# Kernel tuning notes

Measured on AMD Instinct MI355X. Metric: run time of the kernel, lower is better.

Reference implementation:

```python
import jax, jax.numpy as jnp
import numpy as np

N = 50000      # nodes
E = 800000     # edges
F = 256        # input features (glove identity)
H = 64         # hidden dim of GCN stack
C = 16         # num classes
PE = 200000    # pos/neg edges each

@jax.custom_vjp
def grad_reverse(x):
    return x

def _gr_fwd(x):
    return x, None

def _gr_bwd(_, g):
    return (-g,)

grad_reverse.defvjp(_gr_fwd, _gr_bwd)

def _gcn_norm(edge_index, n):
    # add self loops + symmetric normalization (PyG GCNConv default)
    loops = jnp.arange(n, dtype=edge_index.dtype)
    src = jnp.concatenate([edge_index[0], loops])
    dst = jnp.concatenate([edge_index[1], loops])
    deg = jax.ops.segment_sum(jnp.ones(src.shape, jnp.float32), dst, num_segments=n)
    dinv = jnp.where(deg > 0, jax.lax.rsqrt(jnp.maximum(deg, 1.0)), 0.0)
    return src, dst, dinv[src] * dinv[dst]

def _gcn(x, W, b, src, dst, norm, n):
    h = x @ W                                   # [n, out]
    msg = h[src] * norm[:, None]                # gather + edge scale
    return jax.ops.segment_sum(msg, dst, num_segments=n) + b

def setup_inputs():
    key = jax.random.key(0)
    ks = jax.random.split(key, 14)
    s = 0.05
    return {
        "input": jax.random.normal(ks[0], (N, F), jnp.float32),
        "glove": jnp.eye(F, dtype=jnp.float32),
        "W1": jax.random.normal(ks[1], (F, H), jnp.float32) * s,
        "b1": jnp.zeros((H,), jnp.float32),
        "W2": jax.random.normal(ks[2], (H, H), jnp.float32) * s,
        "b2": jnp.zeros((H,), jnp.float32),
        "W3": jax.random.normal(ks[3], (H, H), jnp.float32) * s,
        "b3": jnp.zeros((H,), jnp.float32),
        "Wa": jax.random.normal(ks[4], (H, C), jnp.float32) * s,
        "ba": jnp.zeros((C,), jnp.float32),
        "Wk": jax.random.normal(ks[5], (H, C), jnp.float32) * s,
        "bk": jnp.zeros((C,), jnp.float32),
        "edge_index": jax.random.randint(ks[6], (2, E), 0, N, dtype=jnp.int32),
        "pos_edge_index": jax.random.randint(ks[7], (2, PE), 0, N, dtype=jnp.int32),
        "neg_edge_index": jax.random.randint(ks[8], (2, PE), 0, N, dtype=jnp.int32),
    }

def reference(input, glove, W1, b1, W2, b2, W3, b3, Wa, ba, Wk, bk,
              edge_index, pos_edge_index, neg_edge_index):
    src, dst, norm = _gcn_norm(edge_index, N)
    x = input @ glove
    x = jax.nn.relu(_gcn(x, W1, b1, src, dst, norm, N))
    x = _gcn(x, W2, b2, src, dst, norm, N)
    x = _gcn(x, W3, b3, src, dst, norm, N)
    feat = x
    attr = _gcn(x, Wa, ba, src, dst, norm, N)
    att = _gcn(grad_reverse(x), Wk, bk, src, dst, norm, N)
    tei = jnp.concatenate([pos_edge_index, neg_edge_index], axis=-1)  # [2, 2*PE]
    x_j = x[tei[0]]
    x_i = x[tei[1]]
    res = jnp.einsum('ef,ef->e', x_i, x_j)
    return res, jax.nn.log_softmax(attr, axis=1), att, feat
```

## Files before the change

### kernel.cpp

```cpp
#include <hip/hip_runtime.h>
#include <hip/hip_bf16.h>

#define N_NODES 50000
#define N_EDGES 800000
#define F_IN    256
#define H_DIM   64
#define C_DIM   16
#define PE_CNT  200000

typedef __hip_bfloat16 bf16;

__device__ __forceinline__ float b2f(bf16 v) { return __bfloat162float(v); }
__device__ __forceinline__ bf16  f2b(float v) { return __float2bfloat16(v); }


__global__ void hist_build_kernel(const int* __restrict__ dst, int* __restrict__ hist,
                                  const float* __restrict__ Wa, const float* __restrict__ Wk,
                                  float* __restrict__ Wh) {
    int e = blockIdx.x * blockDim.x + threadIdx.x;
    if (e < N_EDGES) atomicAdd(&hist[dst[e]], 1);
    if (blockIdx.x == 0) {
        for (int idx = threadIdx.x; idx < H_DIM * 32; idx += 256) {
            int f = idx >> 5, c = idx & 31;
            Wh[idx] = (c < C_DIM) ? Wa[f * C_DIM + c] : Wk[f * C_DIM + (c - C_DIM)];
        }
    }
}

__global__ __launch_bounds__(1024) void scan_block_kernel(const int* __restrict__ hist,
                                                          int* __restrict__ excl,
                                                          int* __restrict__ partials) {
    __shared__ int buf[1024];
    int i = blockIdx.x * 1024 + threadIdx.x;
    int v = (i < N_NODES) ? hist[i] : 0;
    buf[threadIdx.x] = v;
    __syncthreads();
    for (int off = 1; off < 1024; off <<= 1) {
        int t = (threadIdx.x >= off) ? buf[threadIdx.x - off] : 0;
        __syncthreads();
        buf[threadIdx.x] += t;
        __syncthreads();
    }
    int incl = buf[threadIdx.x];
    if (i < N_NODES) excl[i] = incl - v;
    if (threadIdx.x == 1023) partials[blockIdx.x] = incl;
}

__global__ void scan_partials_kernel(int* __restrict__ partials) {
    int t = threadIdx.x;
    int orig = (t < 49) ? partials[t] : 0;
    int v = orig;
    for (int off = 1; off < 64; off <<= 1) {
        int u = __shfl_up(v, off, 64);
        if (t >= off) v += u;
    }
    if (t < 49) partials[t] = v - orig;
}

__global__ void scan_add_kernel(int* __restrict__ rowstart, const int* __restrict__ partials,
                                int* __restrict__ cursor, const int* __restrict__ hist,
                                float* __restrict__ dinv) {
    int i = blockIdx.x * blockDim.x + threadIdx.x;
    if (i < N_NODES) {
        int v = rowstart[i] + partials[i >> 10];
        rowstart[i] = v;
        cursor[i]   = v;
        dinv[i]     = rsqrtf((float)(hist[i] + 1));
    } else if (i == N_NODES) {
        rowstart[i] = N_EDGES;
    }
}

__global__ void scatter_kernel(const int* __restrict__ ei, int* __restrict__ cursor,
                               const float* __restrict__ dinv, int2* __restrict__ csr2) {
    int e = blockIdx.x * blockDim.x + threadIdx.x;
    if (e < N_EDGES) {
        int s = ei[e];
        int d = ei[N_EDGES + e];
        int p = atomicAdd(&cursor[d], 1);
        csr2[p] = make_int2(s, __float_as_int(dinv[s]));
    }
}

#define G_ROWS 32
#define G_KCH  64
#define XS_LD  68

__global__ __launch_bounds__(256) void gemm_k256_kernel(const float* __restrict__ x,
                                                        const float* __restrict__ W,
                                                        bf16* __restrict__ h1) {
    __shared__ float xs[G_ROWS * XS_LD];
    __shared__ float ws[G_KCH * H_DIM];
    int t = threadIdx.x;
    int row0 = blockIdx.x * G_ROWS;
    int col = t & 63;
    int wv  = t >> 6;

    float acc[8];
#pragma unroll
    for (int i = 0; i < 8; i++) acc[i] = 0.f;

    for (int c = 0; c < F_IN / G_KCH; c++) {
        int k0 = c * G_KCH;
        {
            const float4* Wg = (const float4*)(W + k0 * H_DIM);
            float4* wl = (float4*)ws;
#pragma unroll
            for (int i = 0; i < 4; i++) wl[t + 256 * i] = Wg[t + 256 * i];
        }
        {
            int r = t >> 3;
            int jj = (t & 7) * 8;
            int row = row0 + r;
            float4 v0 = make_float4(0.f, 0.f, 0.f, 0.f), v1 = v0;
            if (row < N_NODES) {
                const float4* xg = (const float4*)(x + (size_t)row * F_IN + k0 + jj);
                v0 = xg[0];
                v1 = xg[1];
            }
            float4* xl = (float4*)&xs[r * XS_LD + jj];
            xl[0] = v0;
            xl[1] = v1;
        }
        __syncthreads();
#pragma unroll 4
        for (int kk = 0; kk < G_KCH; kk += 4) {
            float w0 = ws[(kk + 0) * H_DIM + col];
            float w1 = ws[(kk + 1) * H_DIM + col];
            float w2 = ws[(kk + 2) * H_DIM + col];
            float w3 = ws[(kk + 3) * H_DIM + col];
#pragma unroll
            for (int i = 0; i < 8; i++) {
                float4 xv = *(const float4*)&xs[(wv * 8 + i) * XS_LD + kk];
                acc[i] += xv.x * w0 + xv.y * w1 + xv.z * w2 + xv.w * w3;
            }
        }
        __syncthreads();
    }
#pragma unroll
    for (int i = 0; i < 8; i++) {
        int row = row0 + wv * 8 + i;
        if (row < N_NODES) h1[(size_t)row * H_DIM + col] = f2b(acc[i]);
    }
}

template <int RELU>
__global__ __launch_bounds__(256) void agg_gemm_kernel(const bf16* __restrict__ h,
                                                       const int* __restrict__ rowstart,
                                                       const int2* __restrict__ csr2,
                                                       const float* __restrict__ dinv,
                                                       const float* __restrict__ bagg,
                                                       const float* __restrict__ W,
                                                       bf16* __restrict__ hnext) {
    int lane = threadIdx.x & 63;
    int node = blockIdx.x * 4 + __builtin_amdgcn_readfirstlane(threadIdx.x >> 6);
    float dn = dinv[node];
    int s0 = rowstart[node], s1 = rowstart[node + 1];
    float acc0 = dn * b2f(h[(size_t)node * H_DIM + lane]);
    float acc1 = 0.f;
    int j = s0;
    for (; j + 1 < s1; j += 2) {
        int2 e0 = csr2[j], e1 = csr2[j + 1];
        acc0 += __int_as_float(e0.y) * b2f(h[(size_t)e0.x * H_DIM + lane]);
        acc1 += __int_as_float(e1.y) * b2f(h[(size_t)e1.x * H_DIM + lane]);
    }
    if (j < s1) {
        int2 e0 = csr2[j];
        acc0 += __int_as_float(e0.y) * b2f(h[(size_t)e0.x * H_DIM + lane]);
    }
    float v = dn * (acc0 + acc1) + bagg[lane];
    if (RELU) v = fmaxf(v, 0.f);
    float o = 0.f;
#pragma unroll
    for (int f = 0; f < H_DIM; f++) {
        float vf = __shfl(v, f, 64);
        o += vf * W[f * H_DIM + lane];
    }
    hnext[(size_t)node * H_DIM + lane] = f2b(o);
}

__global__ __launch_bounds__(256) void agg_out_kernel(const bf16* __restrict__ h,
                                                      const int* __restrict__ rowstart,
                                                      const int2* __restrict__ csr2,
                                                      const float* __restrict__ dinv,
                                                      const float* __restrict__ b3,
                                                      float* __restrict__ feat,
                                                      bf16* __restrict__ featb) {
    int lane = threadIdx.x & 63;
    int node = blockIdx.x * 4 + __builtin_amdgcn_readfirstlane(threadIdx.x >> 6);
    float dn = dinv[node];
    int s0 = rowstart[node], s1 = rowstart[node + 1];
    float acc0 = dn * b2f(h[(size_t)node * H_DIM + lane]);
    float acc1 = 0.f;
    int j = s0;
    for (; j + 1 < s1; j += 2) {
        int2 e0 = csr2[j], e1 = csr2[j + 1];
        acc0 += __int_as_float(e0.y) * b2f(h[(size_t)e0.x * H_DIM + lane]);
        acc1 += __int_as_float(e1.y) * b2f(h[(size_t)e1.x * H_DIM + lane]);
    }
    if (j < s1) {
        int2 e0 = csr2[j];
        acc0 += __int_as_float(e0.y) * b2f(h[(size_t)e0.x * H_DIM + lane]);
    }
    float v = dn * (acc0 + acc1) + b3[lane];
    feat[(size_t)node * H_DIM + lane]  = v;
    featb[(size_t)node * H_DIM + lane] = f2b(v);
}

__global__ __launch_bounds__(256) void head_kernel(const bf16* __restrict__ featb,
                                                   const int* __restrict__ rowstart,
                                                   const int2* __restrict__ csr2,
                                                   const float* __restrict__ dinv,
                                                   const float* __restrict__ Wh,
                                                   const float* __restrict__ ba,
                                                   const float* __restrict__ bk,
                                                   float* __restrict__ lsm,
                                                   float* __restrict__ att) {
    int lane = threadIdx.x & 63;
    int node = blockIdx.x * 4 + __builtin_amdgcn_readfirstlane(threadIdx.x >> 6);
    float dn = dinv[node];
    int s0 = rowstart[node], s1 = rowstart[node + 1];
    float acc0 = dn * b2f(featb[(size_t)node * H_DIM + lane]);
    float acc1 = 0.f;
    int j = s0;
    for (; j + 1 < s1; j += 2) {
        int2 e0 = csr2[j], e1 = csr2[j + 1];
        acc0 += __int_as_float(e0.y) * b2f(featb[(size_t)e0.x * H_DIM + lane]);
        acc1 += __int_as_float(e1.y) * b2f(featb[(size_t)e1.x * H_DIM + lane]);
    }
    if (j < s1) {
        int2 e0 = csr2[j];
        acc0 += __int_as_float(e0.y) * b2f(featb[(size_t)e0.x * H_DIM + lane]);
    }
    float y = dn * (acc0 + acc1);

    int c32 = lane & 31;
    int fbase = lane & 32;
    float part = 0.f;
#pragma unroll
    for (int i = 0; i < 32; i++) {
        float yf = __shfl(y, fbase + i, 64);
        part += yf * Wh[(fbase + i) * 32 + c32];
    }
    float full = part + __shfl(part, lane ^ 32, 64);
    if (lane < 32) {
        float bias = (lane < C_DIM) ? ba[lane] : bk[lane - C_DIM];
        float hv = full + bias;
        if (lane < C_DIM) {
            float m = hv;
#pragma unroll
            for (int off = 1; off < 16; off <<= 1) m = fmaxf(m, __shfl_xor(m, off, 64));
            float e = __expf(hv - m);
            float sum = e;
#pragma unroll
            for (int off = 1; off < 16; off <<= 1) sum += __shfl_xor(sum, off, 64);
            lsm[(size_t)node * C_DIM + lane] = (hv - m) - __logf(sum);
        } else {
            att[(size_t)node * C_DIM + (lane - C_DIM)] = hv;
        }
    }
}

__global__ __launch_bounds__(256) void edge_dot_kernel(const int* __restrict__ pos,
                                                       const int* __restrict__ neg,
                                                       const bf16* __restrict__ xb,
                                                       float* __restrict__ res) {
    int e = blockIdx.x * 16 + (threadIdx.x >> 4);
    int lane = threadIdx.x & 15;
    int a, b;
    if (e < PE_CNT) {
        a = pos[e];
        b = pos[PE_CNT + e];
    } else {
        int e2 = e - PE_CNT;
        a = neg[e2];
        b = neg[PE_CNT + e2];
    }
    uint2 ua = ((const uint2*)(xb + (size_t)a * H_DIM))[lane];
    uint2 ub = ((const uint2*)(xb + (size_t)b * H_DIM))[lane];
    float a0 = __uint_as_float(ua.x << 16), a1 = __uint_as_float(ua.x & 0xffff0000u);
    float a2 = __uint_as_float(ua.y << 16), a3 = __uint_as_float(ua.y & 0xffff0000u);
    float b0 = __uint_as_float(ub.x << 16), b1 = __uint_as_float(ub.x & 0xffff0000u);
    float b2 = __uint_as_float(ub.y << 16), b3 = __uint_as_float(ub.y & 0xffff0000u);
    float acc = a0 * b0 + a1 * b1 + a2 * b2 + a3 * b3;
#pragma unroll
    for (int off = 1; off < 16; off <<= 1) acc += __shfl_xor(acc, off, 64);
    if (lane == 0) res[e] = acc;
}


extern "C" void kernel_launch(void* const* d_in, const int* in_sizes, int n_in,
                              void* d_out, int out_size, void* d_ws, size_t ws_size,
                              hipStream_t stream) {
    const float* input = (const float*)d_in[0];
    const float* W1 = (const float*)d_in[2];
    const float* b1 = (const float*)d_in[3];
    const float* W2 = (const float*)d_in[4];
    const float* b2 = (const float*)d_in[5];
    const float* W3 = (const float*)d_in[6];
    const float* b3 = (const float*)d_in[7];
    const float* Wa = (const float*)d_in[8];
    const float* ba = (const float*)d_in[9];
    const float* Wk = (const float*)d_in[10];
    const float* bk = (const float*)d_in[11];
    const int* ei  = (const int*)d_in[12];
    const int* pos = (const int*)d_in[13];
    const int* neg = (const int*)d_in[14];

    char* ws = (char*)d_ws;
    int*   hist     = (int*)(ws + 0);
    int*   rowstart = (int*)(ws + 200704);
    int*   cursor   = (int*)(ws + 401408);
    float* dinv     = (float*)(ws + 602112);
    int*   partials = (int*)(ws + 802816);
    float* Wh       = (float*)(ws + 803072);
    int2*  csr2     = (int2*)(ws + 811264);
    bf16*  bufA     = (bf16*)(ws + 7211264ULL);
    bf16*  bufB     = (bf16*)(ws + 13611264ULL);

    float* out  = (float*)d_out;
    float* res  = out;
    float* lsm  = out + 400000;
    float* att  = out + 1200000;
    float* feat = out + 2000000;

    hipMemsetAsync(hist, 0, N_NODES * sizeof(int), stream);
    hist_build_kernel<<<(N_EDGES + 255) / 256, 256, 0, stream>>>(ei + N_EDGES, hist, Wa, Wk, Wh);
    scan_block_kernel<<<49, 1024, 0, stream>>>(hist, rowstart, partials);
    scan_partials_kernel<<<1, 64, 0, stream>>>(partials);
    scan_add_kernel<<<196, 256, 0, stream>>>(rowstart, partials, cursor, hist, dinv);
    scatter_kernel<<<(N_EDGES + 255) / 256, 256, 0, stream>>>(ei, cursor, dinv, csr2);

    gemm_k256_kernel<<<(N_NODES + G_ROWS - 1) / G_ROWS, 256, 0, stream>>>(input, W1, bufA);
    agg_gemm_kernel<1><<<12500, 256, 0, stream>>>(bufA, rowstart, csr2, dinv, b1, W2, bufB);
    agg_gemm_kernel<0><<<12500, 256, 0, stream>>>(bufB, rowstart, csr2, dinv, b2, W3, bufA);
    agg_out_kernel<<<12500, 256, 0, stream>>>(bufA, rowstart, csr2, dinv, b3, feat, bufB);
    head_kernel<<<12500, 256, 0, stream>>>(bufB, rowstart, csr2, dinv, Wh, ba, bk, lsm, att);
    edge_dot_kernel<<<25000, 256, 0, stream>>>(pos, neg, bufB, res);
}
```

Measured before the change: 437.0 us.

## Project features before head aggregation, retile GEMM, vectorize gathers and edge dots

Moves the head's 64->32 projection ahead of the final aggregation, so the head kernel gathers 32-wide bf16 rows instead of 64-wide ones and handles two nodes per wavefront. The first GEMM is retiled to a 2x4 register tile per thread with float4 shared-memory reads and packed bf16 stores. Aggregation loops are unrolled by four with paired 128-bit CSR loads, and W is staged in shared memory. The edge dot kernel uses 128-bit loads with 8 lanes per edge. In exchange it adds a bf16 rounding of the projected features and an extra intermediate buffer.

```diff
diff --git a/kernel.cpp b/kernel.cpp
--- a/kernel.cpp
+++ b/kernel.cpp
@@ -12,6 +12,9 @@
 
 __device__ __forceinline__ float b2f(bf16 v) { return __bfloat162float(v); }
 __device__ __forceinline__ bf16  f2b(float v) { return __float2bfloat16(v); }
+__device__ __forceinline__ unsigned short f2b_u(float v) {
+    union { bf16 b; unsigned short u; } cv; cv.b = __float2bfloat16(v); return cv.u;
+}
 
 
 __global__ void hist_build_kernel(const int* __restrict__ dst, int* __restrict__ hist,
@@ -82,6 +85,29 @@
     }
 }
 
+#define AGG_BODY(TBL, STRIDE, CIDX)                                                      \
+    float acc0 = dn * b2f(TBL[(size_t)node * STRIDE + CIDX]);                            \
+    float acc1 = 0.f, acc2 = 0.f, acc3 = 0.f;                                            \
+    int j = s0;                                                                          \
+    if ((j & 1) && j < s1) {                                                             \
+        int2 e = csr2[j];                                                                \
+        acc1 += __int_as_float(e.y) * b2f(TBL[(size_t)e.x * STRIDE + CIDX]);             \
+        j++;                                                                             \
+    }                                                                                    \
+    for (; j + 3 < s1; j += 4) {                                                         \
+        int4 p01 = *(const int4*)&csr2[j];                                               \
+        int4 p23 = *(const int4*)&csr2[j + 2];                                           \
+        acc0 += __int_as_float(p01.y) * b2f(TBL[(size_t)p01.x * STRIDE + CIDX]);         \
+        acc1 += __int_as_float(p01.w) * b2f(TBL[(size_t)p01.z * STRIDE + CIDX]);         \
+        acc2 += __int_as_float(p23.y) * b2f(TBL[(size_t)p23.x * STRIDE + CIDX]);         \
+        acc3 += __int_as_float(p23.w) * b2f(TBL[(size_t)p23.z * STRIDE + CIDX]);         \
+    }                                                                                    \
+    for (; j < s1; j++) {                                                                \
+        int2 e = csr2[j];                                                                \
+        acc0 += __int_as_float(e.y) * b2f(TBL[(size_t)e.x * STRIDE + CIDX]);             \
+    }                                                                                    \
+    float aggsum = (acc0 + acc1) + (acc2 + acc3);
+
 #define G_ROWS 32
 #define G_KCH  64
 #define XS_LD  68
@@ -93,12 +119,11 @@
     __shared__ float ws[G_KCH * H_DIM];
     int t = threadIdx.x;
     int row0 = blockIdx.x * G_ROWS;
-    int col = t & 63;
-    int wv  = t >> 6;
-
-    float acc[8];
-#pragma unroll
-    for (int i = 0; i < 8; i++) acc[i] = 0.f;
+    int c4 = (t & 15) * 4;
+    int r2 = (t >> 4) * 2;
+
+    float acc00 = 0.f, acc01 = 0.f, acc02 = 0.f, acc03 = 0.f;
+    float acc10 = 0.f, acc11 = 0.f, acc12 = 0.f, acc13 = 0.f;
 
     for (int c = 0; c < F_IN / G_KCH; c++) {
         int k0 = c * G_KCH;
@@ -109,8 +134,7 @@
             for (int i = 0; i < 4; i++) wl[t + 256 * i] = Wg[t + 256 * i];
         }
         {
-            int r = t >> 3;
-            int jj = (t & 7) * 8;
+            int r = t >> 3, jj = (t & 7) * 8;
             int row = row0 + r;
             float4 v0 = make_float4(0.f, 0.f, 0.f, 0.f), v1 = v0;
             if (row < N_NODES) {
@@ -123,24 +147,33 @@
             xl[1] = v1;
         }
         __syncthreads();
-#pragma unroll 4
+#pragma unroll 8
         for (int kk = 0; kk < G_KCH; kk += 4) {
-            float w0 = ws[(kk + 0) * H_DIM + col];
-            float w1 = ws[(kk + 1) * H_DIM + col];
-            float w2 = ws[(kk + 2) * H_DIM + col];
-            float w3 = ws[(kk + 3) * H_DIM + col];
-#pragma unroll
-            for (int i = 0; i < 8; i++) {
-                float4 xv = *(const float4*)&xs[(wv * 8 + i) * XS_LD + kk];
-                acc[i] += xv.x * w0 + xv.y * w1 + xv.z * w2 + xv.w * w3;
-            }
+            float4 xv0 = *(const float4*)&xs[(r2 + 0) * XS_LD + kk];
+            float4 xv1 = *(const float4*)&xs[(r2 + 1) * XS_LD + kk];
+            float4 w0 = *(const float4*)&ws[(kk + 0) * H_DIM + c4];
+            float4 w1 = *(const float4*)&ws[(kk + 1) * H_DIM + c4];
+            float4 w2 = *(const float4*)&ws[(kk + 2) * H_DIM + c4];
+            float4 w3 = *(const float4*)&ws[(kk + 3) * H_DIM + c4];
+            acc00 += xv0.x * w0.x + xv0.y * w1.x + xv0.z * w2.x + xv0.w * w3.x;
+            acc01 += xv0.x * w0.y + xv0.y * w1.y + xv0.z * w2.y + xv0.w * w3.y;
+            acc02 += xv0.x * w0.z + xv0.y * w1.z + xv0.z * w2.z + xv0.w * w3.z;
+            acc03 += xv0.x * w0.w + xv0.y * w1.w + xv0.z * w2.w + xv0.w * w3.w;
+            acc10 += xv1.x * w0.x + xv1.y * w1.x + xv1.z * w2.x + xv1.w * w3.x;
+            acc11 += xv1.x * w0.y + xv1.y * w1.y + xv1.z * w2.y + xv1.w * w3.y;
+            acc12 += xv1.x * w0.z + xv1.y * w1.z + xv1.z * w2.z + xv1.w * w3.z;
+            acc13 += xv1.x * w0.w + xv1.y * w1.w + xv1.z * w2.w + xv1.w * w3.w;
         }
         __syncthreads();
     }
-#pragma unroll
-    for (int i = 0; i < 8; i++) {
-        int row = row0 + wv * 8 + i;
-        if (row < N_NODES) h1[(size_t)row * H_DIM + col] = f2b(acc[i]);
+    int rowA = row0 + r2, rowB = rowA + 1;
+    if (rowA < N_NODES) {
+        ushort4 p = make_ushort4(f2b_u(acc00), f2b_u(acc01), f2b_u(acc02), f2b_u(acc03));
+        *(ushort4*)&h1[(size_t)rowA * H_DIM + c4] = p;
+    }
+    if (rowB < N_NODES) {
+        ushort4 p = make_ushort4(f2b_u(acc10), f2b_u(acc11), f2b_u(acc12), f2b_u(acc13));
+        *(ushort4*)&h1[(size_t)rowB * H_DIM + c4] = p;
     }
 }
 
@@ -152,30 +185,26 @@
                                                        const float* __restrict__ bagg,
                                                        const float* __restrict__ W,
                                                        bf16* __restrict__ hnext) {
-    int lane = threadIdx.x & 63;
-    int node = blockIdx.x * 4 + __builtin_amdgcn_readfirstlane(threadIdx.x >> 6);
+    __shared__ float Wl[H_DIM * H_DIM];
+    int t = threadIdx.x;
+    {
+        const float4* Wg = (const float4*)W;
+        float4* wl = (float4*)Wl;
+#pragma unroll
+        for (int i = 0; i < 4; i++) wl[t + 256 * i] = Wg[t + 256 * i];
+    }
+    __syncthreads();
+    int lane = t & 63;
+    int node = blockIdx.x * 4 + __builtin_amdgcn_readfirstlane(t >> 6);
     float dn = dinv[node];
     int s0 = rowstart[node], s1 = rowstart[node + 1];
-    float acc0 = dn * b2f(h[(size_t)node * H_DIM + lane]);
-    float acc1 = 0.f;
-    int j = s0;
-    for (; j + 1 < s1; j += 2) {
-        int2 e0 = csr2[j], e1 = csr2[j + 1];
-        acc0 += __int_as_float(e0.y) * b2f(h[(size_t)e0.x * H_DIM + lane]);
-        acc1 += __int_as_float(e1.y) * b2f(h[(size_t)e1.x * H_DIM + lane]);
-    }
-    if (j < s1) {
-        int2 e0 = csr2[j];
-        acc0 += __int_as_float(e0.y) * b2f(h[(size_t)e0.x * H_DIM + lane]);
-    }
-    float v = dn * (acc0 + acc1) + bagg[lane];
+    AGG_BODY(h, H_DIM, lane)
+    float v = dn * aggsum + bagg[lane];
     if (RELU) v = fmaxf(v, 0.f);
     float o = 0.f;
 #pragma unroll
-    for (int f = 0; f < H_DIM; f++) {
-        float vf = __shfl(v, f, 64);
-        o += vf * W[f * H_DIM + lane];
-    }
+    for (int f = 0; f < H_DIM; f++)
+        o += __shfl(v, f, 64) * Wl[f * H_DIM + lane];
     hnext[(size_t)node * H_DIM + lane] = f2b(o);
 }
 
@@ -184,80 +213,66 @@
                                                       const int2* __restrict__ csr2,
                                                       const float* __restrict__ dinv,
                                                       const float* __restrict__ b3,
+                                                      const float* __restrict__ Wh,
                                                       float* __restrict__ feat,
-                                                      bf16* __restrict__ featb) {
-    int lane = threadIdx.x & 63;
-    int node = blockIdx.x * 4 + __builtin_amdgcn_readfirstlane(threadIdx.x >> 6);
+                                                      bf16* __restrict__ featb,
+                                                      bf16* __restrict__ zb) {
+    __shared__ float Whs[H_DIM * 32];
+    int t = threadIdx.x;
+    {
+        const float4* Wg = (const float4*)Wh;
+        float4* wl = (float4*)Whs;
+#pragma unroll
+        for (int i = 0; i < 2; i++) wl[t + 256 * i] = Wg[t + 256 * i];
+    }
+    __syncthreads();
+    int lane = t & 63;
+    int node = blockIdx.x * 4 + __builtin_amdgcn_readfirstlane(t >> 6);
     float dn = dinv[node];
     int s0 = rowstart[node], s1 = rowstart[node + 1];
-    float acc0 = dn * b2f(h[(size_t)node * H_DIM + lane]);
-    float acc1 = 0.f;
-    int j = s0;
-    for (; j + 1 < s1; j += 2) {
-        int2 e0 = csr2[j], e1 = csr2[j + 1];
-        acc0 += __int_as_float(e0.y) * b2f(h[(size_t)e0.x * H_DIM + lane]);
-        acc1 += __int_as_float(e1.y) * b2f(h[(size_t)e1.x * H_DIM + lane]);
-    }
-    if (j < s1) {
-        int2 e0 = csr2[j];
-        acc0 += __int_as_float(e0.y) * b2f(h[(size_t)e0.x * H_DIM + lane]);
-    }
-    float v = dn * (acc0 + acc1) + b3[lane];
+    AGG_BODY(h, H_DIM, lane)
+    float v = dn * aggsum + b3[lane];
     feat[(size_t)node * H_DIM + lane]  = v;
     featb[(size_t)node * H_DIM + lane] = f2b(v);
-}
-
-__global__ __launch_bounds__(256) void head_kernel(const bf16* __restrict__ featb,
+    int c32 = lane & 31;
+    float zc = 0.f;
+#pragma unroll
+    for (int f = 0; f < H_DIM; f++)
+        zc += __shfl(v, f, 64) * Whs[f * 32 + c32];
+    if (lane < 32) zb[(size_t)node * 32 + lane] = f2b(zc);
+}
+
+__global__ __launch_bounds__(256) void head_kernel(const bf16* __restrict__ zb,
                                                    const int* __restrict__ rowstart,
                                                    const int2* __restrict__ csr2,
                                                    const float* __restrict__ dinv,
-                                                   const float* __restrict__ Wh,
                                                    const float* __restrict__ ba,
                                                    const float* __restrict__ bk,
                                                    float* __restrict__ lsm,
                                                    float* __restrict__ att) {
-    int lane = threadIdx.x & 63;
-    int node = blockIdx.x * 4 + __builtin_amdgcn_readfirstlane(threadIdx.x >> 6);
+    int t = threadIdx.x;
+    int lane = t & 63;
+    int half = lane >> 5;
+    int c32 = lane & 31;
+    int wid = __builtin_amdgcn_readfirstlane(t >> 6);
+    int node = blockIdx.x * 8 + wid * 2 + half;
     float dn = dinv[node];
     int s0 = rowstart[node], s1 = rowstart[node + 1];
-    float acc0 = dn * b2f(featb[(size_t)node * H_DIM + lane]);
-    float acc1 = 0.f;
-    int j = s0;
-    for (; j + 1 < s1; j += 2) {
-        int2 e0 = csr2[j], e1 = csr2[j + 1];
-        acc0 += __int_as_float(e0.y) * b2f(featb[(size_t)e0.x * H_DIM + lane]);
-        acc1 += __int_as_float(e1.y) * b2f(featb[(size_t)e1.x * H_DIM + lane]);
-    }
-    if (j < s1) {
-        int2 e0 = csr2[j];
-        acc0 += __int_as_float(e0.y) * b2f(featb[(size_t)e0.x * H_DIM + lane]);
-    }
-    float y = dn * (acc0 + acc1);
-
-    int c32 = lane & 31;
-    int fbase = lane & 32;
-    float part = 0.f;
-#pragma unroll
-    for (int i = 0; i < 32; i++) {
-        float yf = __shfl(y, fbase + i, 64);
-        part += yf * Wh[(fbase + i) * 32 + c32];
-    }
-    float full = part + __shfl(part, lane ^ 32, 64);
-    if (lane < 32) {
-        float bias = (lane < C_DIM) ? ba[lane] : bk[lane - C_DIM];
-        float hv = full + bias;
-        if (lane < C_DIM) {
-            float m = hv;
-#pragma unroll
-            for (int off = 1; off < 16; off <<= 1) m = fmaxf(m, __shfl_xor(m, off, 64));
-            float e = __expf(hv - m);
-            float sum = e;
-#pragma unroll
-            for (int off = 1; off < 16; off <<= 1) sum += __shfl_xor(sum, off, 64);
-            lsm[(size_t)node * C_DIM + lane] = (hv - m) - __logf(sum);
-        } else {
-            att[(size_t)node * C_DIM + (lane - C_DIM)] = hv;
-        }
+    AGG_BODY(zb, 32, c32)
+    float y = dn * aggsum;
+    int c = c32 & 15;
+    float hv = y + ((c32 < 16) ? ba[c] : bk[c]);
+    if (c32 < 16) {
+        float m = hv;
+#pragma unroll
+        for (int off = 1; off < 16; off <<= 1) m = fmaxf(m, __shfl_xor(m, off, 64));
+        float e = __expf(hv - m);
+        float sum = e;
+#pragma unroll
+        for (int off = 1; off < 16; off <<= 1) sum += __shfl_xor(sum, off, 64);
+        lsm[(size_t)node * C_DIM + c] = (hv - m) - __logf(sum);
+    } else {
+        att[(size_t)node * C_DIM + c] = hv;
     }
 }
 
@@ -265,8 +280,8 @@
                                                        const int* __restrict__ neg,
                                                        const bf16* __restrict__ xb,
                                                        float* __restrict__ res) {
-    int e = blockIdx.x * 16 + (threadIdx.x >> 4);
-    int lane = threadIdx.x & 15;
+    int e = blockIdx.x * 32 + (threadIdx.x >> 3);
+    int lane8 = threadIdx.x & 7;
     int a, b;
     if (e < PE_CNT) {
         a = pos[e];
@@ -276,16 +291,29 @@
         a = neg[e2];
         b = neg[PE_CNT + e2];
     }
-    uint2 ua = ((const uint2*)(xb + (size_t)a * H_DIM))[lane];
-    uint2 ub = ((const uint2*)(xb + (size_t)b * H_DIM))[lane];
-    float a0 = __uint_as_float(ua.x << 16), a1 = __uint_as_float(ua.x & 0xffff0000u);
-    float a2 = __uint_as_float(ua.y << 16), a3 = __uint_as_float(ua.y & 0xffff0000u);
-    float b0 = __uint_as_float(ub.x << 16), b1 = __uint_as_float(ub.x & 0xffff0000u);
-    float b2 = __uint_as_float(ub.y << 16), b3 = __uint_as_float(ub.y & 0xffff0000u);
-    float acc = a0 * b0 + a1 * b1 + a2 * b2 + a3 * b3;
-#pragma unroll
-    for (int off = 1; off < 16; off <<= 1) acc += __shfl_xor(acc, off, 64);
-    if (lane == 0) res[e] = acc;
+    uint4 ua = ((const uint4*)(xb + (size_t)a * H_DIM))[lane8];
+    uint4 ub = ((const uint4*)(xb + (size_t)b * H_DIM))[lane8];
+    float acc;
+    {
+        float s = 0.f;
+        unsigned au, bu;
+        au = ua.x; bu = ub.x;
+        s += __uint_as_float(au << 16) * __uint_as_float(bu << 16);
+        s += __uint_as_float(au & 0xffff0000u) * __uint_as_float(bu & 0xffff0000u);
+        au = ua.y; bu = ub.y;
+        s += __uint_as_float(au << 16) * __uint_as_float(bu << 16);
+        s += __uint_as_float(au & 0xffff0000u) * __uint_as_float(bu & 0xffff0000u);
+        au = ua.z; bu = ub.z;
+        s += __uint_as_float(au << 16) * __uint_as_float(bu << 16);
+        s += __uint_as_float(au & 0xffff0000u) * __uint_as_float(bu & 0xffff0000u);
+        au = ua.w; bu = ub.w;
+        s += __uint_as_float(au << 16) * __uint_as_float(bu << 16);
+        s += __uint_as_float(au & 0xffff0000u) * __uint_as_float(bu & 0xffff0000u);
+        acc = s;
+    }
+#pragma unroll
+    for (int off = 1; off < 8; off <<= 1) acc += __shfl_xor(acc, off, 64);
+    if (lane8 == 0) res[e] = acc;
 }
 
 
@@ -317,6 +345,7 @@
     int2*  csr2     = (int2*)(ws + 811264);
     bf16*  bufA     = (bf16*)(ws + 7211264ULL);
     bf16*  bufB     = (bf16*)(ws + 13611264ULL);
+    bf16*  zb       = (bf16*)(ws + 20011264ULL);
 
     float* out  = (float*)d_out;
     float* res  = out;
@@ -334,7 +363,7 @@
     gemm_k256_kernel<<<(N_NODES + G_ROWS - 1) / G_ROWS, 256, 0, stream>>>(input, W1, bufA);
     agg_gemm_kernel<1><<<12500, 256, 0, stream>>>(bufA, rowstart, csr2, dinv, b1, W2, bufB);
     agg_gemm_kernel<0><<<12500, 256, 0, stream>>>(bufB, rowstart, csr2, dinv, b2, W3, bufA);
-    agg_out_kernel<<<12500, 256, 0, stream>>>(bufA, rowstart, csr2, dinv, b3, feat, bufB);
-    head_kernel<<<12500, 256, 0, stream>>>(bufB, rowstart, csr2, dinv, Wh, ba, bk, lsm, att);
-    edge_dot_kernel<<<25000, 256, 0, stream>>>(pos, neg, bufB, res);
-}
+    agg_out_kernel<<<12500, 256, 0, stream>>>(bufA, rowstart, csr2, dinv, b3, Wh, feat, bufB, zb);
+    head_kernel<<<6250, 256, 0, stream>>>(zb, rowstart, csr2, dinv, ba, bk, lsm, att);
+    edge_dot_kernel<<<12500, 256, 0, stream>>>(pos, neg, bufB, res);
+}
```

Measured after the change: 459.0 us. +5.1%, slower.
